# Optimization experiments

Measured on AMD Instinct MI355X. Metric: run time of the kernel, lower is better.

The kernel has to match this reference:

```python
import jax, jax.numpy as jnp
import numpy as np

H, D, CR, SEL_K = 8, 64, 32, 16          # query heads, head dim, block size, top-k blocks
ROPE_DIM, THETA, WINDOW, GROUPS = 32, 10000.0, 512, 2
INTER, HID, QC = 512, 1024, 256
NEG = -1e30


def _rope_cache(t):
    half = ROPE_DIM // 2
    inv = 1.0 / (THETA ** (jnp.arange(half, dtype=jnp.float32) * 2.0 / ROPE_DIM))
    ang = jnp.arange(t, dtype=jnp.float32)[:, None] * inv[None, :]  # (t, half)
    return jnp.cos(ang), jnp.sin(ang)


def _apply_partial_rope(x, cos, sin):
    half = ROPE_DIM // 2
    x1, x2, rest = x[..., :half], x[..., half:ROPE_DIM], x[..., ROPE_DIM:]
    return jnp.concatenate([x1 * cos - x2 * sin, x1 * sin + x2 * cos, rest], -1)


def _rmsnorm(x, g, eps=1e-6):
    return x * jax.lax.rsqrt(jnp.mean(x * x, -1, keepdims=True) + eps) * g


def setup_inputs():
    key = jax.random.key(0)
    ks = jax.random.split(key, 9)
    f = lambda k, shp, s: jax.random.normal(k, shp, jnp.float32) * s
    return {
        "h": f(ks[0], (1, 2048, HID), 1.0),
        "w_qc": f(ks[1], (HID, QC), QC ** -0.5),
        "w_qup": f(ks[2], (QC, H * D), (H * D) ** -0.5),
        "w_k": f(ks[3], (HID, D), HID ** -0.5),
        "w_v": f(ks[4], (HID, D), HID ** -0.5),
        "g_qnorm": jnp.ones((D,), jnp.float32),
        "g_knorm": jnp.ones((D,), jnp.float32),
        "w_gate": f(ks[5], (D, 3), 0.05),
        "b_gate": jnp.zeros((3,), jnp.float32),
        "sink_logit": f(ks[6], (H,), 0.1),
        "w_out_group": f(ks[7], (GROUPS, (H // GROUPS) * D, INTER), 0.05),
        "w_out": f(ks[8], (GROUPS * INTER, HID), 0.03),
    }


def reference(h, w_qc, w_qup, w_k, w_v, g_qnorm, g_knorm, w_gate, b_gate,
              sink_logit, w_out_group, w_out):
    b, t, _ = h.shape
    cos, sin = _rope_cache(t)
    q = (h @ w_qc @ w_qup).reshape(b, t, H, D).transpose(0, 2, 1, 3)  # (b,H,t,D)
    q = _rmsnorm(_apply_partial_rope(q, cos, sin), g_qnorm)
    k = _rmsnorm(_apply_partial_rope(h @ w_k, cos, sin), g_knorm)      # (b,t,D)
    v = h @ w_v                                                        # (b,t,D)
    scale = 1.0 / np.sqrt(D).astype(np.float32)
    qpos = jnp.arange(t)
    sink = jnp.broadcast_to(sink_logit[None, :, None, None], (b, H, t, 1))

    # ---- compressed branch: attend over block-mean pooled K/V ----
    nb = t // CR
    kc = k[:, :nb * CR].reshape(b, nb, CR, D).mean(2)                  # (b,nb,D)
    vc = v[:, :nb * CR].reshape(b, nb, CR, D).mean(2)
    comp_valid = ((jnp.arange(nb) + 1) * CR - 1)[None, :] <= qpos[:, None]  # (t,nb)
    any_blk = comp_valid.any(-1, keepdims=True)                        # (t,1)
    safe = jnp.where(any_blk, comp_valid, True)
    sc_raw = jnp.einsum('bhqd,bnd->bhqn', q, kc) * scale
    pc = jax.nn.softmax(jnp.concatenate([jnp.where(safe, sc_raw, NEG), sink], -1), -1)
    comp_out = jnp.einsum('bhqn,bnd->bhqd', pc[..., :nb], vc)
    comp_out = jnp.where(any_blk[None, None], comp_out, 0.0)

    # ---- selective branch: top-k blocks per query, dense-masked gather-equivalent ----
    sel_sc = jnp.where(comp_valid, sc_raw, -jnp.inf)
    top_idx = jax.lax.top_k(sel_sc, min(SEL_K, nb))[1]                 # (b,H,t,K)
    sel_blocks = (top_idx[..., :, None] == jnp.arange(nb)).any(-2)     # (b,H,t,nb)
    block_of = jnp.minimum(qpos // CR, nb - 1)
    causal = qpos[:, None] >= qpos[None, :]                            # (t,t)
    in_range = qpos < nb * CR
    tok_sel = sel_blocks[..., block_of] & (causal & in_range[None, :])[None, None]
    scores_full = jnp.einsum('bhqd,bkd->bhqk', q, k) * scale           # (b,H,t,t)
    ps = jax.nn.softmax(jnp.where(tok_sel, scores_full, NEG), -1)
    sel_out = jnp.einsum('bhqk,bkd->bhqd', ps, v)

    # ---- sliding-window branch ----
    sw = causal & ((qpos[:, None] - qpos[None, :]) < WINDOW)
    pw = jax.nn.softmax(
        jnp.concatenate([jnp.where(sw[None, None], scores_full, NEG), sink], -1), -1)
    sw_out = jnp.einsum('bhqk,bkd->bhqd', pw[..., :t], v)

    # ---- learned gate over the three branches ----
    g = jax.nn.sigmoid(q @ w_gate + b_gate)                            # (b,H,t,3)
    g = g / jnp.clip(g.sum(-1, keepdims=True), 1e-6)
    mixed = g[..., 0:1] * comp_out + g[..., 1:2] * sel_out + g[..., 2:3] * sw_out

    # ---- grouped output projection ----
    x = mixed.transpose(0, 2, 1, 3).reshape(b, t, GROUPS, (H // GROUPS) * D)
    y = jnp.einsum('btgf,gfi->btgi', x, w_out_group).reshape(b, t, GROUPS * INTER)
    return y @ w_out
```

## Files before the change

### kernel.cpp

```cpp
#include <hip/hip_runtime.h>
#include <hip/hip_bf16.h>
#include <float.h>
#include <math.h>

typedef __hip_bfloat16 bf16;
typedef float v2f __attribute__((ext_vector_type(2)));

#define NEGBIG (-1e30f)

__device__ __forceinline__ float ldv(const float* p, int i) { return p[i]; }

__device__ __forceinline__ float wave_sum(float v) {
#pragma unroll
  for (int off = 32; off; off >>= 1) v += __shfl_xor(v, off, 64);
  return v;
}
__device__ __forceinline__ float wave_max(float v) {
#pragma unroll
  for (int off = 32; off; off >>= 1) v = fmaxf(v, __shfl_xor(v, off, 64));
  return v;
}

__device__ __forceinline__ float rdlane(float v, int l) {
  return __uint_as_float(__builtin_amdgcn_readlane(__float_as_uint(v), l));
}

template <int L0>
__device__ __forceinline__ void pv16(const float* __restrict__ vp, float e,
                                     float& a0, float& a1, float& a2, float& a3) {
#pragma unroll
  for (int t = 0; t < 16; t += 4) {
    float p0 = rdlane(e, L0 + t + 0);
    float p1 = rdlane(e, L0 + t + 1);
    float p2 = rdlane(e, L0 + t + 2);
    float p3 = rdlane(e, L0 + t + 3);
    a0 += p0 * vp[(t + 0) * 64];
    a1 += p1 * vp[(t + 1) * 64];
    a2 += p2 * vp[(t + 2) * 64];
    a3 += p3 * vp[(t + 3) * 64];
  }
}

__device__ __forceinline__ float qk_dot(const float4* __restrict__ qr,
                                        const float4* __restrict__ kp) {
  v2f d01 = {0.f, 0.f}, d23 = {0.f, 0.f};
#pragma unroll 1
  for (int i = 0; i < 16; i += 2) {
    float4 q0 = qr[i],     k0 = kp[i * 32];
    float4 q1 = qr[i + 1], k1 = kp[i * 32 + 32];
    d01 += (v2f){q0.x, q0.y} * (v2f){k0.x, k0.y};
    d23 += (v2f){q0.z, q0.w} * (v2f){k0.z, k0.w};
    d01 += (v2f){q1.x, q1.y} * (v2f){k1.x, k1.y};
    d23 += (v2f){q1.z, q1.w} * (v2f){k1.z, k1.w};
  }
  v2f d = d01 + d23;
  return d.x + d.y;
}

__device__ __forceinline__ void gemm_core(
    const float* __restrict__ A, const float* __restrict__ B, float* __restrict__ C,
    int K, int lda, int ldb, int ldc, int row0, int col0)
{
  __shared__ __align__(16) float As[2][16][68];
  __shared__ __align__(16) float Bs[2][16][68];
  const int tid = threadIdx.x;
  const int tx = tid & 15, ty = tid >> 4;
  const int ar = tid >> 2;
  const int ak = (tid & 3) * 4;
  const int bk = tid >> 4;
  const int bc = (tid & 15) * 4;

  const int nk = K >> 4;
  float4 a4 = *reinterpret_cast<const float4*>(&A[(row0 + ar) * lda + ak]);
  float4 b4 = *reinterpret_cast<const float4*>(&B[bk * ldb + col0 + bc]);
  {
    As[0][ak + 0][ar] = a4.x; As[0][ak + 1][ar] = a4.y;
    As[0][ak + 2][ar] = a4.z; As[0][ak + 3][ar] = a4.w;
    *reinterpret_cast<float4*>(&Bs[0][bk][bc]) = b4;
  }

  v2f acc01[4] = {};
  v2f acc23[4] = {};
  for (int t = 0; t < nk; ++t) {
    const int cur = t & 1;
    if (t + 1 < nk) {
      int k0 = (t + 1) * 16;
      a4 = *reinterpret_cast<const float4*>(&A[(row0 + ar) * lda + k0 + ak]);
      b4 = *reinterpret_cast<const float4*>(&B[(k0 + bk) * ldb + col0 + bc]);
    }
    __syncthreads();
#pragma unroll
    for (int kk = 0; kk < 16; ++kk) {
      float4 av = *reinterpret_cast<const float4*>(&As[cur][kk][ty * 4]);
      float4 bv = *reinterpret_cast<const float4*>(&Bs[cur][kk][tx * 4]);
      v2f b01; b01.x = bv.x; b01.y = bv.y;
      v2f b23; b23.x = bv.z; b23.y = bv.w;
      float a[4] = {av.x, av.y, av.z, av.w};
#pragma unroll
      for (int i = 0; i < 4; ++i) {
        v2f as; as.x = a[i]; as.y = a[i];
        acc01[i] += as * b01;
        acc23[i] += as * b23;
      }
    }
    if (t + 1 < nk) {
      const int nxt = cur ^ 1;
      As[nxt][ak + 0][ar] = a4.x; As[nxt][ak + 1][ar] = a4.y;
      As[nxt][ak + 2][ar] = a4.z; As[nxt][ak + 3][ar] = a4.w;
      *reinterpret_cast<float4*>(&Bs[nxt][bk][bc]) = b4;
    }
  }
#pragma unroll
  for (int i = 0; i < 4; ++i) {
    float4 o = make_float4(acc01[i].x, acc01[i].y, acc23[i].x, acc23[i].y);
    *reinterpret_cast<float4*>(&C[(row0 + ty * 4 + i) * ldc + col0 + tx * 4]) = o;
  }
}

__global__ __launch_bounds__(256) void gemm_tile(
    const float* __restrict__ A, const float* __restrict__ B, float* __restrict__ C,
    int M, int N, int K, int lda, int ldb, int ldc)
{
  gemm_core(A, B, C, K, lda, ldb, ldc, blockIdx.y * 64, blockIdx.x * 64);
}

__global__ __launch_bounds__(256) void gemm_qckv(
    const float* __restrict__ h, const float* __restrict__ w_qc,
    const float* __restrict__ w_k, const float* __restrict__ w_v,
    float* __restrict__ hc, float* __restrict__ kb, float* __restrict__ vb)
{
  const int x = blockIdx.x;
  if (x < 4) {
    gemm_core(h, w_qc, hc, 1024, 1024, 256, 256, blockIdx.y * 64, x * 64);
  } else if (x == 4) {
    gemm_core(h, w_k, kb, 1024, 1024, 64, 64, blockIdx.y * 64, 0);
  } else {
    gemm_core(h, w_v, vb, 1024, 1024, 64, 64, blockIdx.y * 64, 0);
  }
}

__global__ __launch_bounds__(256) void gemm_dual(
    const float* __restrict__ A0, const float* __restrict__ A1,
    const float* __restrict__ B0, const float* __restrict__ B1,
    float* __restrict__ C0, float* __restrict__ C1,
    int K, int lda, int ldb, int ldc, int nx)
{
  const bool second = (int)blockIdx.x >= nx;
  const float* A = second ? A1 : A0;
  const float* B = second ? B1 : B0;
  float* C = second ? C1 : C0;
  const int bx = second ? (blockIdx.x - nx) : blockIdx.x;
  gemm_core(A, B, C, K, lda, ldb, ldc, blockIdx.y * 64, bx * 64);
}

__global__ __launch_bounds__(256) void rope_table_kernel(float* __restrict__ ct,
                                                         float* __restrict__ st) {
  int tid = blockIdx.x * 256 + threadIdx.x;
  if (tid >= 2048 * 16) return;
  int pos = tid >> 4, i = tid & 15;
  double ang = (double)pos * pow(10000.0, -(double)i / 16.0);
  ct[tid] = (float)cos(ang);
  st[tid] = (float)sin(ang);
}

__device__ __forceinline__ void rope_body(
    float* __restrict__ x, const float* __restrict__ g, int rows, int posShift,
    float* __restrict__ kS, const float* __restrict__ ct, const float* __restrict__ st,
    int bx)
{
  const int lane = threadIdx.x & 63;
  const int wid = threadIdx.x >> 6;
  const int r = bx * 4 + wid;
  if (r >= rows) return;
  const int pos = r >> posShift;
  float val = x[r * 64 + lane];
  float p = __shfl_xor(val, 16, 64);
  float out = val;
  if (lane < 32) {
    int i = lane & 15;
    float cc = ct[pos * 16 + i], ss = st[pos * 16 + i];
    out = (lane < 16) ? (val * cc - p * ss) : (p * ss + val * cc);
  }
  float ms = wave_sum(out * out) * (1.0f / 64.0f);
  float rn = rsqrtf(ms + 1e-6f);
  float res = out * rn * ldv(g, lane);
  x[r * 64 + lane] = res;
  if (kS) {
    int f4 = (r >> 5) * 512 + (lane >> 2) * 32 + (r & 31);
    kS[f4 * 4 + (lane & 3)] = res;
  }
}

__global__ __launch_bounds__(256) void rope_rms_fused(
    float* __restrict__ qx, float* __restrict__ kx,
    const float* __restrict__ gq, const float* __restrict__ gk,
    float* __restrict__ kS, const float* __restrict__ ct, const float* __restrict__ st)
{
  const int bx = blockIdx.x;
  if (bx < 4096) rope_body(qx, gq, 16384, 3, nullptr, ct, st, bx);
  else           rope_body(kx, gk, 2048, 0, kS, ct, st, bx - 4096);
}

__global__ void compress_kernel(const float* __restrict__ k, const float* __restrict__ v,
                                float* __restrict__ kcT4, float* __restrict__ vc)
{
  const int n = blockIdx.x;
  const int d = threadIdx.x;
  float sk = 0.f, sv = 0.f;
  for (int j = 0; j < 32; ++j) {
    sk += k[(n * 32 + j) * 64 + d];
    sv += v[(n * 32 + j) * 64 + d];
  }
  kcT4[(d >> 2) * 256 + n * 4 + (d & 3)] = sk * (1.0f / 32.0f);
  vc[n * 64 + d] = sv * (1.0f / 32.0f);
}

__global__ __launch_bounds__(256) void attn_kernel(
    const float* __restrict__ q, const float* __restrict__ kS, const float* __restrict__ vbuf,
    const float* __restrict__ kcT4, const float* __restrict__ vc,
    const float* __restrict__ w_gate, const float* __restrict__ b_gate,
    const float* __restrict__ sink, float* __restrict__ mixed)
{
  __shared__ __align__(16) float shq[4][64];
  __shared__ int shsel[4][16];
  const int lane = threadIdx.x & 63;
  const int wid = threadIdx.x >> 6;
  const int bid = 4095 - blockIdx.x;
  const int r = bid * 4 + wid;
  const int qpos = r >> 3, h = r & 7;
  const float scale = 0.125f;

  float qv = q[r * 64 + lane];
  shq[wid][lane] = qv;

  float z0 = qv * ldv(w_gate, lane * 3 + 0);
  float z1 = qv * ldv(w_gate, lane * 3 + 1);
  float z2 = qv * ldv(w_gate, lane * 3 + 2);
  z0 = wave_sum(z0) + ldv(b_gate, 0);
  z1 = wave_sum(z1) + ldv(b_gate, 1);
  z2 = wave_sum(z2) + ldv(b_gate, 2);
  float ga0 = 1.f / (1.f + expf(-z0));
  float ga1 = 1.f / (1.f + expf(-z1));
  float ga2 = 1.f / (1.f + expf(-z2));
  float gs = fmaxf(ga0 + ga1 + ga2, 1e-6f);
  float ginv = 1.f / gs;
  ga0 *= ginv; ga1 *= ginv; ga2 *= ginv;

  const float4* qr = reinterpret_cast<const float4*>(&shq[wid][0]);
  const float4* ks4 = reinterpret_cast<const float4*>(kS);
  const float4* kct = reinterpret_cast<const float4*>(kcT4);
  const float snk = ldv(sink, h);
  const int nv = (qpos + 1) >> 5;

  float sc;
  {
    float d0 = 0.f, d1 = 0.f;
#pragma unroll 1
    for (int i = 0; i < 16; i += 2) {
      float4 q0 = qr[i],     k0 = kct[i * 64 + lane];
      float4 q1 = qr[i + 1], k1 = kct[(i + 1) * 64 + lane];
      d0 += q0.x * k0.x + q0.z * k0.z;
      d1 += q0.y * k0.y + q0.w * k0.w;
      d0 += q1.x * k1.x + q1.z * k1.z;
      d1 += q1.y * k1.y + q1.w * k1.w;
    }
    sc = (d0 + d1) * scale;
  }

  float comp_out = 0.f;
  if (nv > 0) {
    float scomp = (lane < nv) ? sc : NEGBIG;
    float m = fmaxf(wave_max(scomp), snk);
    float e = (lane < nv) ? expf(sc - m) : 0.f;
    float S = wave_sum(e) + expf(snk - m);
    float pn = e / S;
    const float* vcp = vc + lane;
    float c0 = 0.f, c1 = 0.f, c2 = 0.f, c3 = 0.f;
    pv16<0>(vcp, pn, c0, c1, c2, c3);
    pv16<16>(vcp + 1024, pn, c0, c1, c2, c3);
    pv16<32>(vcp + 2048, pn, c0, c1, c2, c3);
    pv16<48>(vcp + 3072, pn, c0, c1, c2, c3);
    comp_out = (c0 + c1) + (c2 + c3);
  }

  {
    float selv = (lane < nv) ? sc : -FLT_MAX;
#pragma unroll
    for (int it = 0; it < 16; ++it) {
      float bv = selv; int bi = lane;
#pragma unroll
      for (int off = 32; off; off >>= 1) {
        float ov = __shfl_xor(bv, off, 64);
        int oi = __shfl_xor(bi, off, 64);
        if (ov > bv || (ov == bv && oi < bi)) { bv = ov; bi = oi; }
      }
      if (lane == 0) shsel[wid][it] = bi;
      if (lane == bi) selv = -INFINITY;
    }
  }

  float M = NEGBIG, S = 0.f, osel = 0.f;
#pragma unroll 1
  for (int c = 0; c < 8; ++c) {
    int b0 = shsel[wid][2 * c], b1 = shsel[wid][2 * c + 1];
    int base0 = b0 * 32, base1 = b1 * 32;
    if (base0 > qpos && base1 > qpos) continue;
    int myb = (lane < 32) ? b0 : b1;
    int tok = myb * 32 + (lane & 31);
    bool ok = (tok <= qpos);
    const float4* kp = ks4 + myb * 512 + (lane & 31);
    float s = ok ? qk_dot(qr, kp) * scale : NEGBIG;
    float Mn = fmaxf(M, wave_max(s));
    float e = ok ? expf(s - Mn) : 0.f;
    float cs = wave_sum(e);
    float corr = expf(M - Mn);
    S = S * corr + cs;
    const float* v0 = vbuf + base0 * 64 + lane;
    const float* v1 = vbuf + base1 * 64 + lane;
    float a0 = 0.f, a1 = 0.f, a2 = 0.f, a3 = 0.f;
    pv16<0>(v0, e, a0, a1, a2, a3);
    pv16<16>(v0 + 1024, e, a0, a1, a2, a3);
    pv16<32>(v1, e, a0, a1, a2, a3);
    pv16<48>(v1 + 1024, e, a0, a1, a2, a3);
    osel = osel * corr + ((a0 + a1) + (a2 + a3));
    M = Mn;
  }
  osel /= S;

  float Mw = NEGBIG, Sw = 0.f, osw = 0.f;
  int kstart = qpos - 511; if (kstart < 0) kstart = 0;
  int sbf = kstart >> 5, sbl = qpos >> 5;
#pragma unroll 1
  for (int sb = sbf; sb <= sbl; sb += 2) {
    int sb1 = sb + 1;
    bool v1ok = (sb1 <= sbl);
    int sb1c = v1ok ? sb1 : sb;
    int myb = (lane < 32) ? sb : sb1c;
    int tok = myb * 32 + (lane & 31);
    bool ok = (tok >= kstart) && (tok <= qpos) && ((lane < 32) || v1ok);
    const float4* kp = ks4 + myb * 512 + (lane & 31);
    float s = ok ? qk_dot(qr, kp) * scale : NEGBIG;
    float Mn = fmaxf(Mw, wave_max(s));
    float e = ok ? expf(s - Mn) : 0.f;
    float cs = wave_sum(e);
    float corr = expf(Mw - Mn);
    Sw = Sw * corr + cs;
    const float* v0 = vbuf + sb * 2048 + lane;
    const float* v1 = vbuf + sb1c * 2048 + lane;
    float a0 = 0.f, a1 = 0.f, a2 = 0.f, a3 = 0.f;
    pv16<0>(v0, e, a0, a1, a2, a3);
    pv16<16>(v0 + 1024, e, a0, a1, a2, a3);
    pv16<32>(v1, e, a0, a1, a2, a3);
    pv16<48>(v1 + 1024, e, a0, a1, a2, a3);
    osw = osw * corr + ((a0 + a1) + (a2 + a3));
    Mw = Mn;
  }
  {
    float Mf = fmaxf(Mw, snk);
    float corr = expf(Mw - Mf);
    float Sf = Sw * corr + expf(snk - Mf);
    osw = osw * corr / Sf;
  }

  mixed[r * 64 + lane] = ga0 * comp_out + ga1 * osel + ga2 * osw;
}

extern "C" void kernel_launch(void* const* d_in, const int* in_sizes, int n_in,
                              void* d_out, int out_size, void* d_ws, size_t ws_size,
                              hipStream_t stream) {
  const float* h      = (const float*)d_in[0];
  const float* w_qc   = (const float*)d_in[1];
  const float* w_qup  = (const float*)d_in[2];
  const float* w_k    = (const float*)d_in[3];
  const float* w_v    = (const float*)d_in[4];
  const float* g_qn   = (const float*)d_in[5];
  const float* g_kn   = (const float*)d_in[6];
  const float* w_gate = (const float*)d_in[7];
  const float* b_gate = (const float*)d_in[8];
  const float* sink   = (const float*)d_in[9];
  const float* wog    = (const float*)d_in[10];
  const float* w_out  = (const float*)d_in[11];
  float* out = (float*)d_out;

  float* ws = (float*)d_ws;
  float* hc  = ws;
  float* qb  = hc + 2048 * 256;
  float* kb  = qb + 2048 * 512;
  float* vb  = kb + 2048 * 64;
  float* vc  = vb + 2048 * 64;
  float* mx  = vc + 64 * 64;
  float* y1  = mx + 2048 * 512;
  float* kS  = y1 + 2048 * 1024;
  float* kct4 = kS + 2048 * 64;
  float* ct  = kct4 + 16 * 64 * 4;
  float* st  = ct + 2048 * 16;

  dim3 blk(256);
  rope_table_kernel<<<dim3(128), blk, 0, stream>>>(ct, st);
  gemm_qckv<<<dim3(6, 32), blk, 0, stream>>>(h, w_qc, w_k, w_v, hc, kb, vb);
  gemm_tile<<<dim3(8, 32), blk, 0, stream>>>(hc, w_qup, qb, 2048, 512, 256, 256, 512, 512);
  rope_rms_fused<<<dim3(4608), blk, 0, stream>>>(qb, kb, g_qn, g_kn, kS, ct, st);
  compress_kernel<<<dim3(64), dim3(64), 0, stream>>>(kb, vb, kct4, vc);
  attn_kernel<<<dim3(4096), blk, 0, stream>>>(qb, kS, vb, kct4, vc, w_gate, b_gate, sink, mx);
  gemm_dual<<<dim3(16, 32), blk, 0, stream>>>(mx, mx + 256, wog, wog + 256 * 512,
                                              y1, y1 + 512, 256, 512, 512, 1024, 8);
  gemm_tile<<<dim3(16, 32), blk, 0, stream>>>(y1, w_out, out, 2048, 1024, 1024, 1024, 1024, 1024);
}
```

Measured before the change: 428.8 us.

## Share sliding-window K/V tiles across all heads of a query via LDS

Each attention block now handles one query position with all 8 heads (512 threads), and stages the two 32-token K and V blocks of each sliding-window step into shared memory so all heads reuse them. This is meant to cut redundant global/L2 traffic, since heads share the same K/V. It adds two __syncthreads per iteration and about 32KB of LDS per block, which may lower occupancy. Heads in a block must now advance in lockstep.

Result: faster. 417.2 us (-2.7%).

```diff
diff --git a/kernel.cpp b/kernel.cpp
--- a/kernel.cpp
+++ b/kernel.cpp
@@ -215,19 +215,22 @@
   vc[n * 64 + d] = sv * (1.0f / 32.0f);
 }
 
-__global__ __launch_bounds__(256) void attn_kernel(
+__global__ __launch_bounds__(512) void attn_kernel(
     const float* __restrict__ q, const float* __restrict__ kS, const float* __restrict__ vbuf,
     const float* __restrict__ kcT4, const float* __restrict__ vc,
     const float* __restrict__ w_gate, const float* __restrict__ b_gate,
     const float* __restrict__ sink, float* __restrict__ mixed)
 {
-  __shared__ __align__(16) float shq[4][64];
-  __shared__ int shsel[4][16];
-  const int lane = threadIdx.x & 63;
-  const int wid = threadIdx.x >> 6;
-  const int bid = 4095 - blockIdx.x;
-  const int r = bid * 4 + wid;
-  const int qpos = r >> 3, h = r & 7;
+  __shared__ __align__(16) float4 stgK[1024];
+  __shared__ __align__(16) float stgV[4096];
+  __shared__ __align__(16) float shq[8][64];
+  __shared__ int shsel[8][16];
+  const int tid = threadIdx.x;
+  const int lane = tid & 63;
+  const int wid = tid >> 6;
+  const int qpos = 2047 - blockIdx.x;
+  const int h = wid;
+  const int r = qpos * 8 + h;
   const float scale = 0.125f;
 
   float qv = q[r * 64 + lane];
@@ -251,6 +254,7 @@
   const float4* kct = reinterpret_cast<const float4*>(kcT4);
   const float snk = ldv(sink, h);
   const int nv = (qpos + 1) >> 5;
+
 
   float sc;
   {
@@ -330,23 +334,39 @@
   float Mw = NEGBIG, Sw = 0.f, osw = 0.f;
   int kstart = qpos - 511; if (kstart < 0) kstart = 0;
   int sbf = kstart >> 5, sbl = qpos >> 5;
+  const float4* vbuf4 = reinterpret_cast<const float4*>(vbuf);
 #pragma unroll 1
   for (int sb = sbf; sb <= sbl; sb += 2) {
     int sb1 = sb + 1;
     bool v1ok = (sb1 <= sbl);
     int sb1c = v1ok ? sb1 : sb;
-    int myb = (lane < 32) ? sb : sb1c;
-    int tok = myb * 32 + (lane & 31);
+    __syncthreads();
+#pragma unroll
+    for (int j = 0; j < 2; ++j) {
+      int g = j * 512 + tid;
+      int blk = (g >> 9) ? sb1c : sb;
+      stgK[g] = ks4[blk * 512 + (g & 511)];
+    }
+#pragma unroll
+    for (int j = 0; j < 2; ++j) {
+      int g = j * 512 + tid;
+      int row = g >> 4;
+      int srow = (row < 32) ? (sb * 32 + row) : (sb1c * 32 + (row - 32));
+      reinterpret_cast<float4*>(stgV)[g] = vbuf4[srow * 16 + (g & 15)];
+    }
+    __syncthreads();
+    int myoff = (lane < 32) ? 0 : 512;
+    int tok = ((lane < 32) ? sb : sb1c) * 32 + (lane & 31);
     bool ok = (tok >= kstart) && (tok <= qpos) && ((lane < 32) || v1ok);
-    const float4* kp = ks4 + myb * 512 + (lane & 31);
+    const float4* kp = stgK + myoff + (lane & 31);
     float s = ok ? qk_dot(qr, kp) * scale : NEGBIG;
     float Mn = fmaxf(Mw, wave_max(s));
     float e = ok ? expf(s - Mn) : 0.f;
     float cs = wave_sum(e);
     float corr = expf(Mw - Mn);
     Sw = Sw * corr + cs;
-    const float* v0 = vbuf + sb * 2048 + lane;
-    const float* v1 = vbuf + sb1c * 2048 + lane;
+    const float* v0 = stgV + lane;
+    const float* v1 = stgV + 2048 + lane;
     float a0 = 0.f, a1 = 0.f, a2 = 0.f, a3 = 0.f;
     pv16<0>(v0, e, a0, a1, a2, a3);
     pv16<16>(v0 + 1024, e, a0, a1, a2, a3);
@@ -401,7 +421,7 @@
   gemm_tile<<<dim3(8, 32), blk, 0, stream>>>(hc, w_qup, qb, 2048, 512, 256, 256, 512, 512);
   rope_rms_fused<<<dim3(4608), blk, 0, stream>>>(qb, kb, g_qn, g_kn, kS, ct, st);
   compress_kernel<<<dim3(64), dim3(64), 0, stream>>>(kb, vb, kct4, vc);
-  attn_kernel<<<dim3(4096), blk, 0, stream>>>(qb, kS, vb, kct4, vc, w_gate, b_gate, sink, mx);
+  attn_kernel<<<dim3(2048), dim3(512), 0, stream>>>(qb, kS, vb, kct4, vc, w_gate, b_gate, sink, mx);
   gemm_dual<<<dim3(16, 32), blk, 0, stream>>>(mx, mx + 256, wog, wog + 256 * 512,
                                               y1, y1 + 512, 256, 512, 512, 1024, 8);
   gemm_tile<<<dim3(16, 32), blk, 0, stream>>>(y1, w_out, out, 2048, 1024, 1024, 1024, 1024, 1024);
```
